# Optimization experiments

Measured on AMD Instinct MI355X. Metric: run time of the kernel, lower is better.

The kernel has to match this reference:

```python
import jax, jax.numpy as jnp
import numpy as np

B, S, D, H, HID, NUM_POS = 8, 512, 512, 8, 2048, 1
DIM = D // H
EPS = 1e-3  # keras LayerNormalization default epsilon


def _ln(x, g, b):
    mu = jnp.mean(x, axis=-1, keepdims=True)
    var = jnp.mean(jnp.square(x - mu), axis=-1, keepdims=True)
    return (x - mu) * jax.lax.rsqrt(var + EPS) * g + b


def setup_inputs() -> dict:
    key = jax.random.key(0)
    ks = jax.random.split(key, 12)
    s = 0.02
    return {
        "values": jax.random.normal(ks[0], (B, S, D), jnp.float32),
        "values_mask": jnp.ones((B, S), jnp.bool_),
        "ln0_g": jnp.ones((D,), jnp.float32),
        "ln0_b": jnp.zeros((D,), jnp.float32),
        "W0a": jax.random.normal(ks[1], (D, HID), jnp.float32) * s,
        "b0a": jnp.zeros((HID,), jnp.float32),
        "W0b": jax.random.normal(ks[2], (HID, 3 * D), jnp.float32) * s,
        "b0b": jnp.zeros((3 * D,), jnp.float32),
        "Wp": jax.random.normal(ks[3], (2 * NUM_POS + 1, D), jnp.float32) * s,
        "bp": jnp.zeros((D,), jnp.float32),
        "ln1_g": jnp.ones((D,), jnp.float32),
        "ln1_b": jnp.zeros((D,), jnp.float32),
        "W1a": jax.random.normal(ks[4], (D, HID), jnp.float32) * s,
        "b1a": jnp.zeros((HID,), jnp.float32),
        "W1b": jax.random.normal(ks[5], (HID, D), jnp.float32) * s,
        "b1b": jnp.zeros((D,), jnp.float32),
    }


def reference(values, values_mask, ln0_g, ln0_b, W0a, b0a, W0b, b0b,
              Wp, bp, ln1_g, ln1_b, W1a, b1a, W1b, b1b):
    # Block0: LN -> Dense(HID, relu) -> Dense(3D)  (QKV projection)
    h = _ln(values, ln0_g, ln0_b)
    x = jax.nn.relu(h @ W0a + b0a) @ W0b + b0b            # [B,S,3D]
    x = x.reshape(B, S, H, 3 * DIM).transpose(0, 2, 1, 3)  # [B,H,S,3*dim]
    q, k, v = x[..., :DIM], x[..., DIM:2 * DIM], x[..., 2 * DIM:]

    # relative positions (l2r identity permutation): one-hot(clip(j-i)) @ Wp + bp
    idx = jnp.clip(jnp.arange(S)[None, :] - jnp.arange(S)[:, None],
                   -NUM_POS, NUM_POS) + NUM_POS            # [S,S] in {0,1,2}
    pos = Wp[idx] + bp                                     # [S,S,D]
    pos = pos.reshape(S, S, H, DIM).transpose(2, 0, 1, 3)  # [H,S,S,dim]

    # bias_{bhqk} = q_{bhqd} . pos_{hqkd}
    bias = jnp.einsum('bhqd,hqkd->bhqk', q, pos)

    scores = bias + jnp.einsum('bhqd,bhkd->bhqk', q, k) / jnp.sqrt(
        jnp.asarray(DIM, jnp.float32))

    mask = values_mask[:, None, :, None] & values_mask[:, None, None, :]
    causal = jnp.tril(jnp.ones((S, S), jnp.bool_))
    mask = mask & causal[None, None]
    att = jax.nn.softmax(jnp.where(mask, scores, -999999.0), axis=-1)

    o = jnp.einsum('bhqk,bhkd->bhqd', att, v)              # [B,H,S,dim]
    o = o.transpose(0, 2, 1, 3).reshape(B, S, D)
    values = values + o

    # Block1 FFN residual
    h = _ln(values, ln1_g, ln1_b)
    values = values + (jax.nn.relu(h @ W1a + b1a) @ W1b + b1b)
    return values
```

## Files before the change

### kernel.cpp

```cpp
#include <hip/hip_runtime.h>
#include <hip/hip_bf16.h>
#include <stdint.h>

using hbf = __hip_bfloat16;
typedef __bf16 bf16x8 __attribute__((ext_vector_type(8)));
typedef float f32x4 __attribute__((ext_vector_type(4)));

#define MFMA16(a, b, c) __builtin_amdgcn_mfma_f32_16x16x32_bf16((a), (b), (c), 0, 0, 0)

__device__ __forceinline__ void async_copy16(const void* gsrc, void* ldst) {
  __builtin_amdgcn_global_load_lds((const __attribute__((address_space(1))) void*)gsrc,
                                   (__attribute__((address_space(3))) void*)ldst,
                                   16, 0, 0);
}

__global__ __launch_bounds__(256) void prep_kernel(const float* __restrict__ W0a,
                                                   const float* __restrict__ W0b,
                                                   const float* __restrict__ W1a,
                                                   const float* __restrict__ W1b,
                                                   hbf* __restrict__ T0a, hbf* __restrict__ T0b,
                                                   hbf* __restrict__ T1a, hbf* __restrict__ T1b,
                                                   const float* __restrict__ x,
                                                   const float* __restrict__ g,
                                                   const float* __restrict__ bt,
                                                   hbf* __restrict__ h) {
  const int idx = blockIdx.x;
  const int tid = threadIdx.x;
  if (idx >= 1536) {
    const int row = (idx - 1536) * 4 + (tid >> 6);
    const int l = tid & 63;
    const float* xr = x + (size_t)row * 512;
    float v[8], s = 0.f, s2 = 0.f;
#pragma unroll
    for (int i = 0; i < 8; ++i) {
      float t = xr[l + 64 * i];
      v[i] = t; s += t; s2 += t * t;
    }
#pragma unroll
    for (int off = 32; off; off >>= 1) { s += __shfl_xor(s, off); s2 += __shfl_xor(s2, off); }
    float mu = s * (1.f / 512.f);
    float rs = rsqrtf(s2 * (1.f / 512.f) - mu * mu + 1e-3f);
    hbf* hr = h + (size_t)row * 512;
#pragma unroll
    for (int i = 0; i < 8; ++i) {
      int c = l + 64 * i;
      hr[c] = __float2bfloat16((v[i] - mu) * rs * g[c] + bt[c]);
    }
    return;
  }
  __shared__ float tile[64][65];
  const float* W; hbf* Wt; int K, N, nt, i;
  if (idx < 256)        { W = W0a; Wt = T0a; K = 512;  N = 2048; nt = 32; i = idx; }
  else if (idx < 1024)  { W = W0b; Wt = T0b; K = 2048; N = 1536; nt = 24; i = idx - 256; }
  else if (idx < 1280)  { W = W1a; Wt = T1a; K = 512;  N = 2048; nt = 32; i = idx - 1024; }
  else                  { W = W1b; Wt = T1b; K = 2048; N = 512;  nt = 8;  i = idx - 1280; }
  const int n0 = (i % nt) * 64, k0 = (i / nt) * 64;
#pragma unroll
  for (int t = 0; t < 16; ++t) {
    int q = tid + t * 256;
    int r = q >> 6, c = q & 63;
    tile[r][c] = W[(size_t)(k0 + r) * N + n0 + c];
  }
  __syncthreads();
#pragma unroll
  for (int t = 0; t < 16; ++t) {
    int q = tid + t * 256;
    int r = q >> 6, c = q & 63;
    Wt[(size_t)(n0 + r) * K + k0 + c] = __float2bfloat16(tile[c][r]);
  }
}

__global__ __launch_bounds__(256) void lnadd_kernel(const float* __restrict__ values,
                                                    const float* __restrict__ obuf,
                                                    const float* __restrict__ g,
                                                    const float* __restrict__ bt,
                                                    float* __restrict__ res1,
                                                    hbf* __restrict__ h2) {
  const int row = blockIdx.x * 4 + (threadIdx.x >> 6);
  const int l = threadIdx.x & 63;
  const float* vr = values + (size_t)row * 512;
  const float* orow = obuf + (size_t)row * 512;
  float* rr = res1 + (size_t)row * 512;
  float v[8], s = 0.f, s2 = 0.f;
#pragma unroll
  for (int i = 0; i < 8; ++i) {
    int c = l + 64 * i;
    float t = vr[c] + orow[c];
    v[i] = t; s += t; s2 += t * t;
    rr[c] = t;
  }
#pragma unroll
  for (int off = 32; off; off >>= 1) { s += __shfl_xor(s, off); s2 += __shfl_xor(s2, off); }
  float mu = s * (1.f / 512.f);
  float rs = rsqrtf(s2 * (1.f / 512.f) - mu * mu + 1e-3f);
  hbf* hr = h2 + (size_t)row * 512;
#pragma unroll
  for (int i = 0; i < 8; ++i) {
    int c = l + 64 * i;
    hr[c] = __float2bfloat16((v[i] - mu) * rs * g[c] + bt[c]);
  }
}

template <int EPI, int BN>
__global__ __launch_bounds__(256) void gemm_bt(const hbf* __restrict__ A,
                                               const hbf* __restrict__ Bt,
                                               const float* __restrict__ bias,
                                               const float* __restrict__ resid,
                                               void* __restrict__ outp,
                                               hbf* __restrict__ outp2,
                                               int M, int N, int K) {
  constexpr int WCOLS = (BN == 64) ? 2 : 1;
  constexpr int WROWS = 4 / WCOLS;
  constexpr int MI = 128 / (WROWS * 16);
  constexpr int NJ = BN / (WCOLS * 16);
  constexpr int BCH = BN / 32;
  __shared__ hbf As[2][128 * 64];
  __shared__ hbf Bs[2][BN * 64];
  const int tid = threadIdx.x;
  const int lane = tid & 63;
  const int w = tid >> 6;
  const int wm = w / WCOLS, wn = w % WCOLS;

  const int nbx = gridDim.x;
  const int nwg = nbx * gridDim.y;
  const int bid = blockIdx.y * nbx + blockIdx.x;
  const int cpx = nwg >> 3;
  const int sw = (bid & 7) * cpx + (bid >> 3);
  const int m0 = (sw / nbx) * 128, n0 = (sw % nbx) * BN;

  f32x4 acc[MI][NJ] = {};

  int ar[4], ac[4];
#pragma unroll
  for (int p = 0; p < 4; ++p) {
    int off = p * 4096 + tid * 16;
    int r = off >> 7, sl = (off >> 4) & 7;
    ar[p] = r;
    ac[p] = sl ^ (r & 7);
  }

  auto stage = [&](int buf, int kt) {
#pragma unroll
    for (int p = 0; p < 4; ++p)
      async_copy16(A + (size_t)(m0 + ar[p]) * K + kt + ac[p] * 8,
                   (char*)As[buf] + p * 4096 + tid * 16);
#pragma unroll
    for (int p = 0; p < BCH; ++p)
      async_copy16(Bt + (size_t)(n0 + ar[p]) * K + kt + ac[p] * 8,
                   (char*)Bs[buf] + p * 4096 + tid * 16);
  };

  stage(0, 0);
  int cur = 0;

  for (int kt = 0; kt < K; kt += 64) {
    if (kt + 64 < K) {
      stage(cur ^ 1, kt + 64);
      if constexpr (BN == 64) asm volatile("s_waitcnt vmcnt(6)" ::: "memory");
      else                    asm volatile("s_waitcnt vmcnt(5)" ::: "memory");
    } else {
      asm volatile("s_waitcnt vmcnt(0)" ::: "memory");
    }
    __builtin_amdgcn_s_barrier();
    __builtin_amdgcn_sched_barrier(0);

    const int cq = lane >> 4, lr = lane & 15;
    bf16x8 af[2][MI], bg[2][NJ];
#pragma unroll
    for (int i = 0; i < MI; ++i) {
      int m = wm * (MI * 16) + i * 16 + lr;
#pragma unroll
      for (int kk = 0; kk < 2; ++kk) {
        int sl = (kk * 4 + cq) ^ (m & 7);
        af[kk][i] = *reinterpret_cast<const bf16x8*>((const char*)As[cur] + m * 128 + sl * 16);
      }
    }
#pragma unroll
    for (int j = 0; j < NJ; ++j) {
      int n = wn * (NJ * 16) + j * 16 + lr;
#pragma unroll
      for (int kk = 0; kk < 2; ++kk) {
        int sl = (kk * 4 + cq) ^ (n & 7);
        bg[kk][j] = *reinterpret_cast<const bf16x8*>((const char*)Bs[cur] + n * 128 + sl * 16);
      }
    }
#pragma unroll
    for (int kk = 0; kk < 2; ++kk)
#pragma unroll
      for (int i = 0; i < MI; ++i)
#pragma unroll
        for (int j = 0; j < NJ; ++j)
          acc[i][j] = MFMA16(af[kk][i], bg[kk][j], acc[i][j]);

    __builtin_amdgcn_sched_barrier(0);
    __builtin_amdgcn_s_barrier();
    cur ^= 1;
  }

  const int lr = lane & 15;
  if (EPI == 3 && (n0 % 192) >= 128) {
    const int hh = n0 / 192;
#pragma unroll
    for (int j = 0; j < NJ; ++j) {
      int col = n0 + wn * (NJ * 16) + j * 16 + lr;
      int d = (col % 192) - 128;
      float bcol = bias[col];
#pragma unroll
      for (int i = 0; i < MI; ++i) {
        int rowb = m0 + wm * (MI * 16) + i * 16 + (lane >> 4) * 4;
        int bb_ = rowb >> 9, s0 = rowb & 511;
        unsigned short u[4];
#pragma unroll
        for (int r = 0; r < 4; ++r) {
          hbf t = __float2bfloat16(acc[i][j][r] + bcol);
          u[r] = *reinterpret_cast<unsigned short*>(&t);
        }
        uint2 pk;
        pk.x = (unsigned)u[0] | ((unsigned)u[1] << 16);
        pk.y = (unsigned)u[2] | ((unsigned)u[3] << 16);
        *reinterpret_cast<uint2*>(outp2 + ((size_t)(bb_ * 8 + hh) * 64 + d) * 512 + s0) = pk;
      }
    }
    return;
  }

#pragma unroll
  for (int j = 0; j < NJ; ++j) {
    int col = n0 + wn * (NJ * 16) + j * 16 + lr;
    float bcol = bias[col];
#pragma unroll
    for (int i = 0; i < MI; ++i) {
      int rowb = m0 + wm * (MI * 16) + i * 16 + (lane >> 4) * 4;
#pragma unroll
      for (int r = 0; r < 4; ++r) {
        int row = rowb + r;
        float v = acc[i][j][r] + bcol;
        if (EPI == 0) {
          v = v > 0.f ? v : 0.f;
          ((hbf*)outp)[(size_t)row * N + col] = __float2bfloat16(v);
        } else if (EPI == 1 || EPI == 3) {
          ((hbf*)outp)[(size_t)row * N + col] = __float2bfloat16(v);
        } else {
          ((float*)outp)[(size_t)row * N + col] = v + resid[(size_t)row * N + col];
        }
      }
    }
  }
}

__global__ __launch_bounds__(256) void attn_kernel(const hbf* __restrict__ X2,
                                                   const hbf* __restrict__ vT,
                                                   const float* __restrict__ Wp,
                                                   const float* __restrict__ bp,
                                                   float* __restrict__ obuf) {
  __shared__ float bias_lds[2][64];
  __shared__ hbf p_lds[4][16][32];
  const int wid = blockIdx.y * 64 + blockIdx.x;
  const int bh = ((wid & 7) << 3) | ((wid >> 3) & 7);
  const int q0 = (wid >> 6) * 64;
  const int b = bh >> 3, h = bh & 7;
  const int tid = threadIdx.x;
  const int lane = tid & 63, w = tid >> 6;
  const int qbase = q0 + w * 16;

  if (tid < 128) {
    int c = tid >> 6, qq = tid & 63;
    const hbf* qp = X2 + (size_t)(b * 512 + q0 + qq) * 1536 + h * 192;
    const float* wr = Wp + c * 512 + h * 64;
    const float* br = bp + h * 64;
    float s = 0.f;
#pragma unroll
    for (int d8 = 0; d8 < 8; ++d8) {
      bf16x8 qv = *reinterpret_cast<const bf16x8*>(qp + d8 * 8);
#pragma unroll
      for (int j = 0; j < 8; ++j) s += (float)qv[j] * (wr[d8 * 8 + j] + br[d8 * 8 + j]);
    }
    bias_lds[c][qq] = s;
  }

  bf16x8 qa[2];
  {
    int qrow = qbase + (lane & 15);
    const hbf* qp = X2 + (size_t)(b * 512 + qrow) * 1536 + h * 192 + (lane >> 4) * 8;
#pragma unroll
    for (int c = 0; c < 2; ++c) qa[c] = *reinterpret_cast<const bf16x8*>(qp + c * 32);
  }
  __syncthreads();

  float bias0[4], bias1[4];
#pragma unroll
  for (int r = 0; r < 4; ++r) {
    int qq = w * 16 + (lane >> 4) * 4 + r;
    bias0[r] = bias_lds[0][qq];
    bias1[r] = bias_lds[1][qq];
  }

  const float MAXS = 16.f;
  float lsum[4] = {0.f, 0.f, 0.f, 0.f};
  f32x4 oacc[4];
#pragma unroll
  for (int nt = 0; nt < 4; ++nt) oacc[nt] = (f32x4){0.f, 0.f, 0.f, 0.f};

  const int qhi = qbase + 15;
  const int nchunks = (qhi >> 5) + 1;
  for (int ch = 0; ch < nchunks; ++ch) {
    const int k32 = ch * 32;
    f32x4 z = {0.f, 0.f, 0.f, 0.f};
    f32x4 s0, s1;
    {
      const hbf* kp = X2 + (size_t)(b * 512 + k32 + (lane & 15)) * 1536 + h * 192 + 64 + (lane >> 4) * 8;
      bf16x8 kb = *reinterpret_cast<const bf16x8*>(kp);
      s0 = MFMA16(qa[0], kb, z);
      kb = *reinterpret_cast<const bf16x8*>(kp + 32);
      s0 = MFMA16(qa[1], kb, s0);
      const hbf* kp1 = kp + 16 * 1536;
      kb = *reinterpret_cast<const bf16x8*>(kp1);
      s1 = MFMA16(qa[0], kb, z);
      kb = *reinterpret_cast<const bf16x8*>(kp1 + 32);
      s1 = MFMA16(qa[1], kb, s1);
    }
    const int col0 = k32 + (lane & 15);
    const int col1 = col0 + 16;
#pragma unroll
    for (int r = 0; r < 4; ++r) {
      int q = qbase + (lane >> 4) * 4 + r;
      float sc0 = (col0 > q) ? -1e30f : (s0[r] * 0.125f + (col0 == q ? bias1[r] : bias0[r]));
      float sc1 = (col1 > q) ? -1e30f : (s1[r] * 0.125f + (col1 == q ? bias1[r] : bias0[r]));
      float p0 = __expf(sc0 - MAXS);
      float p1 = __expf(sc1 - MAXS);
      lsum[r] += p0 + p1;
      p_lds[w][(lane >> 4) * 4 + r][lane & 15] = __float2bfloat16(p0);
      p_lds[w][(lane >> 4) * 4 + r][16 + (lane & 15)] = __float2bfloat16(p1);
    }
    bf16x8 pa = *reinterpret_cast<const bf16x8*>(&p_lds[w][lane & 15][(lane >> 4) * 8]);
#pragma unroll
    for (int nt = 0; nt < 4; ++nt) {
      const hbf* vp = vT + ((size_t)bh * 64 + nt * 16 + (lane & 15)) * 512 + k32 + (lane >> 4) * 8;
      bf16x8 vb = *reinterpret_cast<const bf16x8*>(vp);
      oacc[nt] = MFMA16(pa, vb, oacc[nt]);
    }
  }
#pragma unroll
  for (int r = 0; r < 4; ++r) {
#pragma unroll
    for (int off = 1; off < 16; off <<= 1) lsum[r] += __shfl_xor(lsum[r], off);
    float rl = 1.f / lsum[r];
    int q = qbase + (lane >> 4) * 4 + r;
    float* orow = obuf + (size_t)(b * 512 + q) * 512 + h * 64;
#pragma unroll
    for (int nt = 0; nt < 4; ++nt) orow[nt * 16 + (lane & 15)] = oacc[nt][r] * rl;
  }
}

extern "C" void kernel_launch(void* const* d_in, const int* in_sizes, int n_in,
                              void* d_out, int out_size, void* d_ws, size_t ws_size,
                              hipStream_t stream) {
  const float* values = (const float*)d_in[0];
  const float* ln0_g = (const float*)d_in[2];
  const float* ln0_b = (const float*)d_in[3];
  const float* W0a = (const float*)d_in[4];
  const float* b0a = (const float*)d_in[5];
  const float* W0b = (const float*)d_in[6];
  const float* b0b = (const float*)d_in[7];
  const float* Wp = (const float*)d_in[8];
  const float* bp = (const float*)d_in[9];
  const float* ln1_g = (const float*)d_in[10];
  const float* ln1_b = (const float*)d_in[11];
  const float* W1a = (const float*)d_in[12];
  const float* b1a = (const float*)d_in[13];
  const float* W1b = (const float*)d_in[14];
  const float* b1b = (const float*)d_in[15];

  char* ws = (char*)d_ws;
  hbf* W0a_t = (hbf*)(ws + (0ull << 20));
  hbf* W0b_t = (hbf*)(ws + (2ull << 20));
  hbf* W1a_t = (hbf*)(ws + (8ull << 20));
  hbf* W1b_t = (hbf*)(ws + (10ull << 20));
  hbf* hbuf = (hbf*)(ws + (12ull << 20));
  hbf* X1 = (hbf*)(ws + (16ull << 20));
  hbf* X2 = (hbf*)(ws + (32ull << 20));
  float* obuf = (float*)(ws + (44ull << 20));
  hbf* vT = (hbf*)(ws + (52ull << 20));
  float* res1 = (float*)(ws + (57ull << 20));
  hbf* X3 = X1;
  hbf* h2 = hbuf;

  prep_kernel<<<2560, 256, 0, stream>>>(W0a, W0b, W1a, W1b, W0a_t, W0b_t, W1a_t, W1b_t,
                                        values, ln0_g, ln0_b, hbuf);

  gemm_bt<0, 64><<<dim3(32, 32), 256, 0, stream>>>(hbuf, W0a_t, b0a, nullptr, X1, nullptr, 4096, 2048, 512);
  gemm_bt<3, 64><<<dim3(24, 32), 256, 0, stream>>>(X1, W0b_t, b0b, nullptr, X2, vT, 4096, 1536, 2048);

  attn_kernel<<<dim3(64, 8), 256, 0, stream>>>(X2, vT, Wp, bp, obuf);

  lnadd_kernel<<<1024, 256, 0, stream>>>(values, obuf, ln1_g, ln1_b, res1, h2);

  gemm_bt<0, 64><<<dim3(32, 32), 256, 0, stream>>>(h2, W1a_t, b1a, nullptr, X3, nullptr, 4096, 2048, 512);
  gemm_bt<2, 32><<<dim3(16, 32), 256, 0, stream>>>(X3, W1b_t, b1b, res1, (float*)d_out, nullptr, 4096, 512, 2048);
}
```

Before: 226.4 us.

## Load GEMM B operand directly to registers and store attention output in bf16

The GEMM kernel stops staging the B (weight) tile through shared memory. Each wave now computes 32 rows by the full BN columns and loads its B fragments straight from global memory into registers, double-buffered one k-step ahead, with the k loop unrolled by two. This removes LDS traffic and footprint for B, but each of the four waves now fetches the whole B tile separately and register pressure rises. Separately, the attention output buffer is written and read as bf16 instead of fp32, halving that round trip at some cost in precision.

Result: slower. 353.1 us (+56.0%).

```diff
diff --git a/kernel.cpp b/kernel.cpp
--- a/kernel.cpp
+++ b/kernel.cpp
@@ -71,7 +71,7 @@
 }
 
 __global__ __launch_bounds__(256) void lnadd_kernel(const float* __restrict__ values,
-                                                    const float* __restrict__ obuf,
+                                                    const hbf* __restrict__ obuf,
                                                     const float* __restrict__ g,
                                                     const float* __restrict__ bt,
                                                     float* __restrict__ res1,
@@ -79,13 +79,13 @@
   const int row = blockIdx.x * 4 + (threadIdx.x >> 6);
   const int l = threadIdx.x & 63;
   const float* vr = values + (size_t)row * 512;
-  const float* orow = obuf + (size_t)row * 512;
+  const hbf* orow = obuf + (size_t)row * 512;
   float* rr = res1 + (size_t)row * 512;
   float v[8], s = 0.f, s2 = 0.f;
 #pragma unroll
   for (int i = 0; i < 8; ++i) {
     int c = l + 64 * i;
-    float t = vr[c] + orow[c];
+    float t = vr[c] + __bfloat162float(orow[c]);
     v[i] = t; s += t; s2 += t * t;
     rr[c] = t;
   }
@@ -109,17 +109,13 @@
                                                void* __restrict__ outp,
                                                hbf* __restrict__ outp2,
                                                int M, int N, int K) {
-  constexpr int WCOLS = (BN == 64) ? 2 : 1;
-  constexpr int WROWS = 4 / WCOLS;
-  constexpr int MI = 128 / (WROWS * 16);
-  constexpr int NJ = BN / (WCOLS * 16);
-  constexpr int BCH = BN / 32;
+  constexpr int MI = 2;
+  constexpr int NJ = BN / 16;
   __shared__ hbf As[2][128 * 64];
-  __shared__ hbf Bs[2][BN * 64];
   const int tid = threadIdx.x;
   const int lane = tid & 63;
   const int w = tid >> 6;
-  const int wm = w / WCOLS, wn = w % WCOLS;
+  const int cq = lane >> 4, lr = lane & 15;
 
   const int nbx = gridDim.x;
   const int nwg = nbx * gridDim.y;
@@ -144,70 +140,73 @@
     for (int p = 0; p < 4; ++p)
       async_copy16(A + (size_t)(m0 + ar[p]) * K + kt + ac[p] * 8,
                    (char*)As[buf] + p * 4096 + tid * 16);
-#pragma unroll
-    for (int p = 0; p < BCH; ++p)
-      async_copy16(Bt + (size_t)(n0 + ar[p]) * K + kt + ac[p] * 8,
-                   (char*)Bs[buf] + p * 4096 + tid * 16);
   };
 
-  stage(0, 0);
-  int cur = 0;
-
-  for (int kt = 0; kt < K; kt += 64) {
+  int boff[NJ];
+#pragma unroll
+  for (int j = 0; j < NJ; ++j) boff[j] = (n0 + j * 16 + lr) * K + cq * 8;
+
+  auto loadB = [&](bf16x8 (&bg)[2][NJ], int kt) {
+#pragma unroll
+    for (int kk = 0; kk < 2; ++kk)
+#pragma unroll
+      for (int j = 0; j < NJ; ++j)
+        bg[kk][j] = *reinterpret_cast<const bf16x8*>(Bt + boff[j] + kt + kk * 32);
+  };
+
+  bf16x8 bg0[2][NJ], bg1[2][NJ];
+
+  auto kstep = [&](int buf, int kt, bf16x8 (&bgCur)[2][NJ], bf16x8 (&bgNext)[2][NJ]) {
     if (kt + 64 < K) {
-      stage(cur ^ 1, kt + 64);
-      if constexpr (BN == 64) asm volatile("s_waitcnt vmcnt(6)" ::: "memory");
-      else                    asm volatile("s_waitcnt vmcnt(5)" ::: "memory");
+      stage(buf ^ 1, kt + 64);
+      loadB(bgNext, kt + 64);
+      if constexpr (BN == 64) asm volatile("s_waitcnt vmcnt(12)" ::: "memory");
+      else                    asm volatile("s_waitcnt vmcnt(8)" ::: "memory");
     } else {
       asm volatile("s_waitcnt vmcnt(0)" ::: "memory");
     }
     __builtin_amdgcn_s_barrier();
     __builtin_amdgcn_sched_barrier(0);
 
-    const int cq = lane >> 4, lr = lane & 15;
-    bf16x8 af[2][MI], bg[2][NJ];
+    bf16x8 af[2][MI];
 #pragma unroll
     for (int i = 0; i < MI; ++i) {
-      int m = wm * (MI * 16) + i * 16 + lr;
+      int m = w * 32 + i * 16 + lr;
 #pragma unroll
       for (int kk = 0; kk < 2; ++kk) {
         int sl = (kk * 4 + cq) ^ (m & 7);
-        af[kk][i] = *reinterpret_cast<const bf16x8*>((const char*)As[cur] + m * 128 + sl * 16);
+        af[kk][i] = *reinterpret_cast<const bf16x8*>((const char*)As[buf] + m * 128 + sl * 16);
       }
     }
 #pragma unroll
-    for (int j = 0; j < NJ; ++j) {
-      int n = wn * (NJ * 16) + j * 16 + lr;
-#pragma unroll
-      for (int kk = 0; kk < 2; ++kk) {
-        int sl = (kk * 4 + cq) ^ (n & 7);
-        bg[kk][j] = *reinterpret_cast<const bf16x8*>((const char*)Bs[cur] + n * 128 + sl * 16);
-      }
-    }
-#pragma unroll
     for (int kk = 0; kk < 2; ++kk)
 #pragma unroll
       for (int i = 0; i < MI; ++i)
 #pragma unroll
         for (int j = 0; j < NJ; ++j)
-          acc[i][j] = MFMA16(af[kk][i], bg[kk][j], acc[i][j]);
+          acc[i][j] = MFMA16(af[kk][i], bgCur[kk][j], acc[i][j]);
 
     __builtin_amdgcn_sched_barrier(0);
     __builtin_amdgcn_s_barrier();
-    cur ^= 1;
-  }
-
-  const int lr = lane & 15;
+  };
+
+  stage(0, 0);
+  loadB(bg0, 0);
+  for (int kt = 0; kt < K; kt += 128) {
+    kstep(0, kt, bg0, bg1);
+    kstep(1, kt + 64, bg1, bg0);
+  }
+
   if (EPI == 3 && (n0 % 192) >= 128) {
     const int hh = n0 / 192;
 #pragma unroll
     for (int j = 0; j < NJ; ++j) {
-      int col = n0 + wn * (NJ * 16) + j * 16 + lr;
+      int col = n0 + j * 16 + lr;
       int d = (col % 192) - 128;
       float bcol = bias[col];
 #pragma unroll
       for (int i = 0; i < MI; ++i) {
-        int rowb = m0 + wm * (MI * 16) + i * 16 + (lane >> 4) * 4;
+        int rowb = m0 + w * 32 + i * 16 + cq * 4;
         int bb_ = rowb >> 9, s0 = rowb & 511;
         unsigned short u[4];
 #pragma unroll
@@ -226,11 +225,11 @@
 
 #pragma unroll
   for (int j = 0; j < NJ; ++j) {
-    int col = n0 + wn * (NJ * 16) + j * 16 + lr;
+    int col = n0 + j * 16 + lr;
     float bcol = bias[col];
 #pragma unroll
     for (int i = 0; i < MI; ++i) {
-      int rowb = m0 + wm * (MI * 16) + i * 16 + (lane >> 4) * 4;
+      int rowb = m0 + w * 32 + i * 16 + cq * 4;
 #pragma unroll
       for (int r = 0; r < 4; ++r) {
         int row = rowb + r;
@@ -252,7 +251,7 @@
                                                    const hbf* __restrict__ vT,
                                                    const float* __restrict__ Wp,
                                                    const float* __restrict__ bp,
-                                                   float* __restrict__ obuf) {
+                                                   hbf* __restrict__ obuf) {
   __shared__ float bias_lds[2][64];
   __shared__ hbf p_lds[4][16][32];
   const int wid = blockIdx.y * 64 + blockIdx.x;
@@ -346,9 +345,9 @@
     for (int off = 1; off < 16; off <<= 1) lsum[r] += __shfl_xor(lsum[r], off);
     float rl = 1.f / lsum[r];
     int q = qbase + (lane >> 4) * 4 + r;
-    float* orow = obuf + (size_t)(b * 512 + q) * 512 + h * 64;
-#pragma unroll
-    for (int nt = 0; nt < 4; ++nt) orow[nt * 16 + (lane & 15)] = oacc[nt][r] * rl;
+    hbf* orow = obuf + (size_t)(b * 512 + q) * 512 + h * 64;
+#pragma unroll
+    for (int nt = 0; nt < 4; ++nt) orow[nt * 16 + (lane & 15)] = __float2bfloat16(oacc[nt][r] * rl);
   }
 }
 
@@ -379,7 +378,7 @@
   hbf* hbuf = (hbf*)(ws + (12ull << 20));
   hbf* X1 = (hbf*)(ws + (16ull << 20));
   hbf* X2 = (hbf*)(ws + (32ull << 20));
-  float* obuf = (float*)(ws + (44ull << 20));
+  hbf* obuf = (hbf*)(ws + (44ull << 20));
   hbf* vT = (hbf*)(ws + (52ull << 20));
   float* res1 = (float*)(ws + (57ull << 20));
   hbf* X3 = X1;
```
